# Kernel optimization log

Measured on AMD Instinct MI355X. Metric: run time of the kernel, lower is better.

The kernel has to match this reference:

```python
import jax, jax.numpy as jnp
import numpy as np

B, S, D, H = 4, 1024, 512, 8
EPS = 1e-5


def _cx(x):
    # [..., 2] float -> complex
    return jax.lax.complex(x[..., 0], x[..., 1])


def setup_inputs() -> dict:
    key = jax.random.key(0)
    ks = jax.random.split(key, 9)
    f = lambda k, sh: jax.random.normal(k, sh, dtype=jnp.float32)
    inp = {
        "q": f(ks[0], (B, S, D, 2)),
        "k": f(ks[1], (B, S, D, 2)),
        "v": f(ks[2], (B, S, D, 2)),
        "Wq": f(ks[3], (D, D, 2)) * 0.02,
        "bq": f(ks[4], (D, 2)) * 0.02,
        "Wk": f(ks[5], (D, D, 2)) * 0.02,
        "bk": f(ks[6], (D, 2)) * 0.02,
        "Wv": f(ks[7], (D, D, 2)) * 0.02,
        "bv": f(ks[8], (D, 2)) * 0.02,
        "gamma_r": jnp.ones((D,), jnp.float32),
        "beta_r": jnp.zeros((D,), jnp.float32),
        "gamma_i": jnp.ones((D,), jnp.float32),
        "beta_i": jnp.zeros((D,), jnp.float32),
        "n_heads": H,
    }
    return inp


def _layernorm(x, g, b):
    # torch LayerNorm: biased variance, eps inside sqrt
    mu = jnp.mean(x, axis=-1, keepdims=True)
    var = jnp.mean((x - mu) ** 2, axis=-1, keepdims=True)
    return (x - mu) / jnp.sqrt(var + EPS) * g + b


def reference(q, k, v, Wq, bq, Wk, bk, Wv, bv, gamma_r, beta_r, gamma_i, beta_i, n_heads):
    qc, kc, vc = _cx(q), _cx(k), _cx(v)
    # complex linear: x @ W^T + b
    Q = jnp.einsum("bsd,ed->bse", qc, _cx(Wq)) + _cx(bq)
    K = jnp.einsum("bsd,ed->bse", kc, _cx(Wk)) + _cx(bk)
    V = jnp.einsum("bsd,ed->bse", vc, _cx(Wv)) + _cx(bv)
    b, s, d = qc.shape
    dh = d // n_heads
    Qh = Q.reshape(b, s, n_heads, dh)
    Kh = K.reshape(b, s, n_heads, dh)
    Vh = V.reshape(b, s, n_heads, dh)
    # complex scores [b,h,q,k], scaled by sqrt(dh)
    scores = jnp.einsum("bqhd,bkhd->bhqk", Qh, Kh) / jnp.sqrt(jnp.float32(dh))
    # original: softmax over view_as_real dim=-2 == key axis, real & imag independently
    attn = jax.lax.complex(jax.nn.softmax(scores.real, axis=-1),
                           jax.nn.softmax(scores.imag, axis=-1))
    # (dropout is identity in eval mode)
    out = jnp.einsum("bhqk,bkhd->bqhd", attn, Vh).reshape(b, s, d)
    out = out + qc  # residual
    out_r = _layernorm(out.real, gamma_r, beta_r)
    out_i = _layernorm(out.imag, gamma_i, beta_i)
    return jnp.stack([out_r, out_i], axis=-1)  # [B,S,D,2]
```

## Files before the change

kernel.cpp:

```cpp
#include <hip/hip_runtime.h>
#include <math.h>

#define BB  4
#define SS  1024
#define DD  512
#define HH  8
#define DHD 64
#define PL  2097152
#define WPL 262144

constexpr float LN_EPS = 1e-5f;

using half4 = __attribute__((ext_vector_type(4))) _Float16;
using half8 = __attribute__((ext_vector_type(8))) _Float16;
using f32x4 = __attribute__((ext_vector_type(4))) float;

__device__ __forceinline__ half8 negh(half8 a) {
    union { half8 h; unsigned int u[4]; } t;
    t.h = a;
    #pragma unroll
    for (int i = 0; i < 4; ++i) t.u[i] ^= 0x80008000u;
    return t.h;
}
__device__ __forceinline__ half8 ldh64(const unsigned short* p, int row, int col) {
    return *(const half8*)(p + row * 64 + (col ^ ((row & 7) << 3)));
}
#define MFMA16(acc, a, b) acc = __builtin_amdgcn_mfma_f32_16x16x32_f16(a, b, acc, 0, 0, 0)

__global__ __launch_bounds__(256)
void cvt_kernel(const float2* __restrict__ s0, const float2* __restrict__ s1,
                const float2* __restrict__ s2, unsigned short* __restrict__ dst,
                int planeElems) {
    const int z = blockIdx.y;
    const float2* src = z == 0 ? s0 : (z == 1 ? s1 : s2);
    unsigned short* base = dst + (size_t)z * 2 * planeElems;
    const int idx = (blockIdx.x * 256 + threadIdx.x) * 2;
    float4 t = *(const float4*)(src + idx);
    union { _Float16 h[2]; unsigned int u; } r, i;
    r.h[0] = (_Float16)t.x; r.h[1] = (_Float16)t.z;
    i.h[0] = (_Float16)t.y; i.h[1] = (_Float16)t.w;
    ((unsigned int*)(base))[idx >> 1] = r.u;
    ((unsigned int*)(base + planeElems))[idx >> 1] = i.u;
}

__global__ __launch_bounds__(256, 1)
void proj_kernel(const unsigned short* __restrict__ XP,
                 const unsigned short* __restrict__ WP,
                 const float2* __restrict__ bq, const float2* __restrict__ bk,
                 const float2* __restrict__ bv,
                 unsigned short* __restrict__ QG, unsigned short* __restrict__ KG,
                 unsigned short* __restrict__ VG) {
    const unsigned short* XR = XP + (size_t)blockIdx.z * 2 * PL;
    const unsigned short* XI = XR + PL;
    const unsigned short* WRp = WP + (size_t)blockIdx.z * 2 * WPL;
    const unsigned short* WIp = WRp + WPL;
    const float2* bias; unsigned short* outP;
    if (blockIdx.z == 0)      { bias = bq; outP = QG; }
    else if (blockIdx.z == 1) { bias = bk; outP = KG; }
    else                      { bias = bv; outP = VG; }
    const bool isV = (blockIdx.z == 2);

    __shared__ __align__(16) unsigned short Xs[2][2][128 * 64];
    __shared__ __align__(16) unsigned short Ws[2][2][128 * 64];

    const int tid  = threadIdx.x;
    const int w    = tid >> 6;
    const int lane = tid & 63;
    const int quad = lane >> 4;
    const int l15  = lane & 15;
    const int wm   = w >> 1;
    const int we   = w & 1;
    const int m0   = blockIdx.x * 128;
    const int e0   = blockIdx.y * 128;

    const int srow = lane >> 3;
    const int sg   = lane & 7;
    const int scol = ((sg ^ srow) << 3);
    const unsigned short* gplane;
    unsigned short* l0p; unsigned short* l1p;
    int row0;
    if (w == 0)      { gplane = XR;  row0 = m0; l0p = &Xs[0][0][0]; l1p = &Xs[1][0][0]; }
    else if (w == 1) { gplane = XI;  row0 = m0; l0p = &Xs[0][1][0]; l1p = &Xs[1][1][0]; }
    else if (w == 2) { gplane = WRp; row0 = e0; l0p = &Ws[0][0][0]; l1p = &Ws[1][0][0]; }
    else             { gplane = WIp; row0 = e0; l0p = &Ws[0][1][0]; l1p = &Ws[1][1][0]; }
    const unsigned short* gs = gplane + (size_t)(row0 + srow) * DD + scol;

#define STAGE(LB, DC) { \
        const unsigned short* _g = gs + (DC); \
        _Pragma("unroll") \
        for (int j = 0; j < 16; ++j) \
            __builtin_amdgcn_global_load_lds( \
                (const __attribute__((address_space(1))) void*)(_g + j * 8 * DD), \
                (__attribute__((address_space(3))) void*)((LB) + j * 512), \
                16, 0, 0); \
    }

    f32x4 Sr[4][4], Si[4][4];
    #pragma unroll
    for (int a = 0; a < 4; ++a)
        #pragma unroll
        for (int c = 0; c < 4; ++c) { Sr[a][c] = (f32x4)0.f; Si[a][c] = (f32x4)0.f; }

    STAGE(l0p, 0);
    __syncthreads();

    #pragma unroll 2
    for (int s = 0; s < 8; ++s) {
        if (s < 7) STAGE(((s & 1) ? l0p : l1p), (s + 1) * 64);

        const unsigned short* xb0 = &Xs[s & 1][0][0];
        const unsigned short* xb1 = &Xs[s & 1][1][0];
        const unsigned short* wb0 = &Ws[s & 1][0][0];
        const unsigned short* wb1 = &Ws[s & 1][1][0];

        #pragma unroll
        for (int kc = 0; kc < 2; ++kc) {
            const int dl = kc * 32 + quad * 8;
            half8 xr[4], xi[4];
            #pragma unroll
            for (int mf = 0; mf < 4; ++mf) {
                const int mr = wm * 64 + mf * 16 + l15;
                xr[mf] = ldh64(xb0, mr, dl);
                xi[mf] = ldh64(xb1, mr, dl);
            }
            #pragma unroll
            for (int ef = 0; ef < 4; ++ef) {
                const int er = we * 64 + ef * 16 + l15;
                half8 wr  = ldh64(wb0, er, dl);
                half8 wi  = ldh64(wb1, er, dl);
                half8 wmi = negh(wi);
                #pragma unroll
                for (int mf = 0; mf < 4; ++mf) {
                    MFMA16(Sr[mf][ef], xr[mf], wr);
                    MFMA16(Sr[mf][ef], xi[mf], wmi);
                    MFMA16(Si[mf][ef], xr[mf], wi);
                    MFMA16(Si[mf][ef], xi[mf], wr);
                }
            }
        }
        __syncthreads();
    }
#undef STAGE

    #pragma unroll
    for (int ef = 0; ef < 4; ++ef) {
        const int eg  = e0 + we * 64 + ef * 16 + l15;
        const int hh  = eg >> 6;
        const int col = eg & 63;
        float2 bb = bias[eg];
        #pragma unroll
        for (int mf = 0; mf < 4; ++mf) {
            #pragma unroll
            for (int reg = 0; reg < 4; ++reg) {
                int m = m0 + wm * 64 + mf * 16 + quad * 4 + reg;
                int bidx = m >> 10;
                int sidx = m & 1023;
                int bh = bidx * HH + hh;
                union { _Float16 h; unsigned short u; } cr, ci;
                cr.h = (_Float16)(Sr[mf][ef][reg] + bb.x);
                ci.h = (_Float16)(Si[mf][ef][reg] + bb.y);
                size_t o = isV ? ((size_t)bh * DHD + col) * SS + sidx
                               : ((size_t)bh * SS + sidx) * DHD + col;
                outP[0 * PL + o] = cr.u;
                outP[1 * PL + o] = ci.u;
            }
        }
    }
}

#define AWID 72
__global__ __launch_bounds__(256, 2)
void attn_kernel(const unsigned short* __restrict__ QG, const unsigned short* __restrict__ KG,
                 const unsigned short* __restrict__ VG,
                 unsigned short* __restrict__ ObR, unsigned short* __restrict__ ObI) {
    __shared__ unsigned short Ks[2][64 * AWID];
    __shared__ unsigned short Vt[2][64 * AWID];
    __shared__ unsigned short Ps[2][64 * AWID];
    __shared__ float lbuf[2][2][64];

    const int n   = blockIdx.x;
    const int bh  = (n & 7) * 4 + (n >> 7);
    const int q0  = ((n >> 3) & 15) * 64;
    const int b   = bh >> 3;
    const int h   = bh & 7;

    const int tid  = threadIdx.x;
    const int w    = tid >> 6;
    const int lane = tid & 63;
    const int quad = lane >> 4;
    const int l15  = lane & 15;
    const int sw   = w & 1;
    const int tw   = w >> 1;

    half8 qfr[2][2], qfi[2][2], qfmi[2][2];
    #pragma unroll
    for (int qt = 0; qt < 2; ++qt)
        #pragma unroll
        for (int kc = 0; kc < 2; ++kc) {
            size_t qa = ((size_t)bh * SS + q0 + sw * 32 + qt * 16 + l15) * DHD + kc * 32 + quad * 8;
            qfr[qt][kc]  = *(const half8*)(QG + qa);
            qfi[qt][kc]  = *(const half8*)(QG + PL + qa);
            qfmi[qt][kc] = negh(qfi[qt][kc]);
        }

    f32x4 acc[2][2][4];
    #pragma unroll
    for (int qt = 0; qt < 2; ++qt)
        #pragma unroll
        for (int dt = 0; dt < 2; ++dt)
            #pragma unroll
            for (int p = 0; p < 4; ++p) acc[qt][dt][p] = (f32x4)0.f;
    float lacc[2][2] = {{0.f, 0.f}, {0.f, 0.f}};

    const int srow = tid >> 3;
    const int sg   = (tid & 7) * 8;

    for (int kt = 0; kt < SS; kt += 64) {
        __syncthreads();
        #pragma unroll
        for (int p = 0; p < 2; ++p)
            #pragma unroll
            for (int it = 0; it < 2; ++it) {
                const int r = it * 32 + srow;
                *(uint4*)&Ks[p][r * AWID + sg] =
                    *(const uint4*)(KG + (size_t)p * PL + ((size_t)bh * SS + kt + r) * DHD + sg);
                *(uint4*)&Vt[p][r * AWID + sg] =
                    *(const uint4*)(VG + (size_t)p * PL + ((size_t)bh * DHD + r) * SS + kt + sg);
            }
        __syncthreads();

        f32x4 Sr[2][2], Si[2][2];
        #pragma unroll
        for (int a = 0; a < 2; ++a)
            #pragma unroll
            for (int c = 0; c < 2; ++c) { Sr[a][c] = (f32x4)0.f; Si[a][c] = (f32x4)0.f; }
        #pragma unroll
        for (int kc = 0; kc < 2; ++kc) {
            #pragma unroll
            for (int kt2 = 0; kt2 < 2; ++kt2) {
                const int krow = tw * 32 + kt2 * 16 + l15;
                half8 akr = *(const half8*)&Ks[0][krow * AWID + kc * 32 + quad * 8];
                half8 aki = *(const half8*)&Ks[1][krow * AWID + kc * 32 + quad * 8];
                #pragma unroll
                for (int qt = 0; qt < 2; ++qt) {
                    MFMA16(Sr[kt2][qt], akr, qfr[qt][kc]);
                    MFMA16(Sr[kt2][qt], aki, qfmi[qt][kc]);
                    MFMA16(Si[kt2][qt], aki, qfr[qt][kc]);
                    MFMA16(Si[kt2][qt], akr, qfi[qt][kc]);
                }
            }
        }

        #pragma unroll
        for (int kt2 = 0; kt2 < 2; ++kt2)
            #pragma unroll
            for (int qt = 0; qt < 2; ++qt) {
                half4 pr, pi;
                float sr_ = 0.f, si_ = 0.f;
                #pragma unroll
                for (int reg = 0; reg < 4; ++reg) {
                    float er = __expf(Sr[kt2][qt][reg] * 0.125f);
                    float ei = __expf(Si[kt2][qt][reg] * 0.125f);
                    pr[reg] = (_Float16)er;
                    pi[reg] = (_Float16)ei;
                    sr_ += (float)pr[reg];
                    si_ += (float)pi[reg];
                }
                lacc[qt][0] += sr_;
                lacc[qt][1] += si_;
                const int qrow = sw * 32 + qt * 16 + l15;
                const int kcol = tw * 32 + kt2 * 16 + quad * 4;
                *(half4*)&Ps[0][qrow * AWID + kcol] = pr;
                *(half4*)&Ps[1][qrow * AWID + kcol] = pi;
            }
        __syncthreads();

        #pragma unroll
        for (int kc = 0; kc < 2; ++kc) {
            half8 ap[2][2];
            #pragma unroll
            for (int qt = 0; qt < 2; ++qt) {
                const int qrow = sw * 32 + qt * 16 + l15;
                ap[qt][0] = *(const half8*)&Ps[0][qrow * AWID + kc * 32 + quad * 8];
                ap[qt][1] = *(const half8*)&Ps[1][qrow * AWID + kc * 32 + quad * 8];
            }
            #pragma unroll
            for (int dt = 0; dt < 2; ++dt) {
                const int drow = tw * 32 + dt * 16 + l15;
                half8 bvr = *(const half8*)&Vt[0][drow * AWID + kc * 32 + quad * 8];
                half8 bvi = *(const half8*)&Vt[1][drow * AWID + kc * 32 + quad * 8];
                #pragma unroll
                for (int qt = 0; qt < 2; ++qt) {
                    MFMA16(acc[qt][dt][0], ap[qt][0], bvr);
                    MFMA16(acc[qt][dt][1], ap[qt][0], bvi);
                    MFMA16(acc[qt][dt][2], ap[qt][1], bvr);
                    MFMA16(acc[qt][dt][3], ap[qt][1], bvi);
                }
            }
        }
    }

    __syncthreads();
    #pragma unroll
    for (int qt = 0; qt < 2; ++qt)
        #pragma unroll
        for (int p = 0; p < 2; ++p) {
            float v = lacc[qt][p];
            v += __shfl_xor(v, 16);
            v += __shfl_xor(v, 32);
            if (lane < 16) lbuf[p][tw][sw * 32 + qt * 16 + lane] = v;
        }
    __syncthreads();

    #pragma unroll
    for (int qt = 0; qt < 2; ++qt)
        #pragma unroll
        for (int reg = 0; reg < 4; ++reg) {
            const int qloc = sw * 32 + qt * 16 + quad * 4 + reg;
            const float ir = 1.f / (lbuf[0][0][qloc] + lbuf[0][1][qloc]);
            const float ii = 1.f / (lbuf[1][0][qloc] + lbuf[1][1][qloc]);
            #pragma unroll
            for (int dt = 0; dt < 2; ++dt) {
                const int d = tw * 32 + dt * 16 + l15;
                union { _Float16 h; unsigned short u; } cr, ci;
                cr.h = (_Float16)(acc[qt][dt][0][reg] * ir - acc[qt][dt][3][reg] * ii);
                ci.h = (_Float16)(acc[qt][dt][1][reg] * ir + acc[qt][dt][2][reg] * ii);
                size_t o = ((size_t)b * SS + q0 + qloc) * DD + h * DHD + d;
                ObR[o] = cr.u;
                ObI[o] = ci.u;
            }
        }
}

__global__ __launch_bounds__(256)
void ln_kernel(const unsigned short* __restrict__ OrP, const unsigned short* __restrict__ OiP,
               const float2* __restrict__ Qin,
               const float* __restrict__ gr, const float* __restrict__ br,
               const float* __restrict__ gi, const float* __restrict__ bi,
               float2* __restrict__ out) {
    const int row = blockIdx.x;
    const int tid = threadIdx.x;
    const size_t base = (size_t)row * DD;
    const int e0 = 2 * tid, e1 = 2 * tid + 1;

    union { unsigned int u; _Float16 h[2]; } tr, ti;
    tr.u = *(const unsigned int*)(OrP + base + e0);
    ti.u = *(const unsigned int*)(OiP + base + e0);
    float2 r0 = Qin[base + e0];
    float2 r1 = Qin[base + e1];
    float xr0 = (float)tr.h[0] + r0.x;
    float xr1 = (float)tr.h[1] + r1.x;
    float xi0 = (float)ti.h[0] + r0.y;
    float xi1 = (float)ti.h[1] + r1.y;

    float sr = xr0 + xr1;
    float si = xi0 + xi1;
    float qr = xr0 * xr0 + xr1 * xr1;
    float qi = xi0 * xi0 + xi1 * xi1;
    #pragma unroll
    for (int off = 32; off > 0; off >>= 1) {
        sr += __shfl_down(sr, off);
        si += __shfl_down(si, off);
        qr += __shfl_down(qr, off);
        qi += __shfl_down(qi, off);
    }
    __shared__ float red[4][4];
    __shared__ float stat[4];
    int lane = tid & 63, wid = tid >> 6;
    if (lane == 0) { red[wid][0] = sr; red[wid][1] = si; red[wid][2] = qr; red[wid][3] = qi; }
    __syncthreads();
    if (tid == 0) {
        sr = red[0][0] + red[1][0] + red[2][0] + red[3][0];
        si = red[0][1] + red[1][1] + red[2][1] + red[3][1];
        qr = red[0][2] + red[1][2] + red[2][2] + red[3][2];
        qi = red[0][3] + red[1][3] + red[2][3] + red[3][3];
        float mur = sr * (1.f / DD), mui = si * (1.f / DD);
        float vr = qr * (1.f / DD) - mur * mur;
        float vi = qi * (1.f / DD) - mui * mui;
        stat[0] = mur; stat[1] = mui;
        stat[2] = rsqrtf(vr + LN_EPS); stat[3] = rsqrtf(vi + LN_EPS);
    }
    __syncthreads();
    float mur = stat[0], mui = stat[1], rsr = stat[2], rsi = stat[3];
    out[base + e0] = make_float2((xr0 - mur) * rsr * gr[e0] + br[e0],
                                 (xi0 - mui) * rsi * gi[e0] + bi[e0]);
    out[base + e1] = make_float2((xr1 - mur) * rsr * gr[e1] + br[e1],
                                 (xi1 - mui) * rsi * gi[e1] + bi[e1]);
}

extern "C" void kernel_launch(void* const* d_in, const int* in_sizes, int n_in,
                              void* d_out, int out_size, void* d_ws, size_t ws_size,
                              hipStream_t stream) {
    const float2* q  = (const float2*)d_in[0];
    const float2* k  = (const float2*)d_in[1];
    const float2* v  = (const float2*)d_in[2];
    const float2* Wq = (const float2*)d_in[3];
    const float2* bq = (const float2*)d_in[4];
    const float2* Wk = (const float2*)d_in[5];
    const float2* bk = (const float2*)d_in[6];
    const float2* Wv = (const float2*)d_in[7];
    const float2* bv = (const float2*)d_in[8];
    const float*  gr = (const float*)d_in[9];
    const float*  br = (const float*)d_in[10];
    const float*  gi = (const float*)d_in[11];
    const float*  bi = (const float*)d_in[12];

    unsigned short* XP  = (unsigned short*)d_ws;
    unsigned short* WP  = XP + (size_t)6 * PL;
    unsigned short* QG  = WP + (size_t)6 * WPL;
    unsigned short* KG  = QG + (size_t)2 * PL;
    unsigned short* VG  = KG + (size_t)2 * PL;
    unsigned short* ObR = VG + (size_t)2 * PL;
    unsigned short* ObI = ObR + (size_t)PL;

    cvt_kernel<<<dim3(4096, 3), 256, 0, stream>>>(q, k, v, XP, PL);
    cvt_kernel<<<dim3(512, 3), 256, 0, stream>>>(Wq, Wk, Wv, WP, WPL);
    proj_kernel<<<dim3(32, 4, 3), 256, 0, stream>>>(XP, WP, bq, bk, bv, QG, KG, VG);
    attn_kernel<<<dim3(512), 256, 0, stream>>>(QG, KG, VG, ObR, ObI);
    ln_kernel<<<dim3(BB * SS), 256, 0, stream>>>(ObR, ObI, q, gr, br, gi, bi, (float2*)d_out);
}
```

Baseline: 216.7 us.

## Store fp16 planes in 128x64 tiles and single-buffer the projection GEMM for two blocks per CU

```diff
diff --git a/kernel.cpp b/kernel.cpp
--- a/kernel.cpp
+++ b/kernel.cpp
@@ -36,14 +36,17 @@
     unsigned short* base = dst + (size_t)z * 2 * planeElems;
     const int idx = (blockIdx.x * 256 + threadIdx.x) * 2;
     float4 t = *(const float4*)(src + idx);
+    const int m = idx >> 9;
+    const int d = idx & 511;
+    const int ob = (((m >> 7) << 3) + (d >> 6)) * 8192 + ((m & 127) << 6) + (d & 63);
     union { _Float16 h[2]; unsigned int u; } r, i;
     r.h[0] = (_Float16)t.x; r.h[1] = (_Float16)t.z;
     i.h[0] = (_Float16)t.y; i.h[1] = (_Float16)t.w;
-    ((unsigned int*)(base))[idx >> 1] = r.u;
-    ((unsigned int*)(base + planeElems))[idx >> 1] = i.u;
-}
-
-__global__ __launch_bounds__(256, 1)
+    *(unsigned int*)(base + ob) = r.u;
+    *(unsigned int*)(base + planeElems + ob) = i.u;
+}
+
+__global__ __launch_bounds__(256, 2)
 void proj_kernel(const unsigned short* __restrict__ XP,
                  const unsigned short* __restrict__ WP,
                  const float2* __restrict__ bq, const float2* __restrict__ bk,
@@ -60,8 +63,8 @@
     else                      { bias = bv; outP = VG; }
     const bool isV = (blockIdx.z == 2);
 
-    __shared__ __align__(16) unsigned short Xs[2][2][128 * 64];
-    __shared__ __align__(16) unsigned short Ws[2][2][128 * 64];
+    __shared__ __align__(16) unsigned short Xs[2][128 * 64];
+    __shared__ __align__(16) unsigned short Ws[2][128 * 64];
 
     const int tid  = threadIdx.x;
     const int w    = tid >> 6;
@@ -75,25 +78,14 @@
 
     const int srow = lane >> 3;
     const int sg   = lane & 7;
-    const int scol = ((sg ^ srow) << 3);
     const unsigned short* gplane;
-    unsigned short* l0p; unsigned short* l1p;
+    unsigned short* lb;
     int row0;
-    if (w == 0)      { gplane = XR;  row0 = m0; l0p = &Xs[0][0][0]; l1p = &Xs[1][0][0]; }
-    else if (w == 1) { gplane = XI;  row0 = m0; l0p = &Xs[0][1][0]; l1p = &Xs[1][1][0]; }
-    else if (w == 2) { gplane = WRp; row0 = e0; l0p = &Ws[0][0][0]; l1p = &Ws[1][0][0]; }
-    else             { gplane = WIp; row0 = e0; l0p = &Ws[0][1][0]; l1p = &Ws[1][1][0]; }
-    const unsigned short* gs = gplane + (size_t)(row0 + srow) * DD + scol;
-
-#define STAGE(LB, DC) { \
-        const unsigned short* _g = gs + (DC); \
-        _Pragma("unroll") \
-        for (int j = 0; j < 16; ++j) \
-            __builtin_amdgcn_global_load_lds( \
-                (const __attribute__((address_space(1))) void*)(_g + j * 8 * DD), \
-                (__attribute__((address_space(3))) void*)((LB) + j * 512), \
-                16, 0, 0); \
-    }
+    if (w == 0)      { gplane = XR;  row0 = m0; lb = &Xs[0][0]; }
+    else if (w == 1) { gplane = XI;  row0 = m0; lb = &Xs[1][0]; }
+    else if (w == 2) { gplane = WRp; row0 = e0; lb = &Ws[0][0]; }
+    else             { gplane = WIp; row0 = e0; lb = &Ws[1][0]; }
+    const unsigned short* gs = gplane + (size_t)row0 * DD + srow * 64 + ((sg ^ srow) << 3);
 
     f32x4 Sr[4][4], Si[4][4];
     #pragma unroll
@@ -101,17 +93,16 @@
         #pragma unroll
         for (int c = 0; c < 4; ++c) { Sr[a][c] = (f32x4)0.f; Si[a][c] = (f32x4)0.f; }
 
-    STAGE(l0p, 0);
-    __syncthreads();
-
-    #pragma unroll 2
     for (int s = 0; s < 8; ++s) {
-        if (s < 7) STAGE(((s & 1) ? l0p : l1p), (s + 1) * 64);
-
-        const unsigned short* xb0 = &Xs[s & 1][0][0];
-        const unsigned short* xb1 = &Xs[s & 1][1][0];
-        const unsigned short* wb0 = &Ws[s & 1][0][0];
-        const unsigned short* wb1 = &Ws[s & 1][1][0];
+        if (s) __syncthreads();
+        const unsigned short* _g = gs + (size_t)s * 8192;
+        #pragma unroll
+        for (int j = 0; j < 16; ++j)
+            __builtin_amdgcn_global_load_lds(
+                (const __attribute__((address_space(1))) void*)(_g + j * 512),
+                (__attribute__((address_space(3))) void*)(lb + j * 512),
+                16, 0, 0);
+        __syncthreads();
 
         #pragma unroll
         for (int kc = 0; kc < 2; ++kc) {
@@ -120,14 +111,14 @@
             #pragma unroll
             for (int mf = 0; mf < 4; ++mf) {
                 const int mr = wm * 64 + mf * 16 + l15;
-                xr[mf] = ldh64(xb0, mr, dl);
-                xi[mf] = ldh64(xb1, mr, dl);
+                xr[mf] = ldh64(Xs[0], mr, dl);
+                xi[mf] = ldh64(Xs[1], mr, dl);
             }
             #pragma unroll
             for (int ef = 0; ef < 4; ++ef) {
                 const int er = we * 64 + ef * 16 + l15;
-                half8 wr  = ldh64(wb0, er, dl);
-                half8 wi  = ldh64(wb1, er, dl);
+                half8 wr  = ldh64(Ws[0], er, dl);
+                half8 wi  = ldh64(Ws[1], er, dl);
                 half8 wmi = negh(wi);
                 #pragma unroll
                 for (int mf = 0; mf < 4; ++mf) {
@@ -138,9 +129,7 @@
                 }
             }
         }
-        __syncthreads();
     }
-#undef STAGE
 
     #pragma unroll
     for (int ef = 0; ef < 4; ++ef) {
```

New measurement: 207.4 us. -4.3%, faster.
